# Kernel optimization log

Hardware: AMD Instinct MI355X
Metric: run time of the kernel (lower is better)

Reference implementation:

```python
import jax, jax.numpy as jnp
import numpy as np
import math

EMBED_DIM = 4096
NUM_HEADS = 32
NUM_KV_HEADS = 8
HEAD_DIM = EMBED_DIM // NUM_HEADS          # 128
GROUP_SIZE = NUM_HEADS // NUM_KV_HEADS     # 4
KV_DIM = EMBED_DIM // GROUP_SIZE           # 1024
BATCH, SEQ = 1, 2048


def softermax(x, axis=-1):
    # base-2 softmax with max subtraction (Softermax, arXiv:2103.09301)
    m = jnp.max(x, axis=axis, keepdims=True)
    p = jnp.exp2(x - m)
    return p / jnp.sum(p, axis=axis, keepdims=True)


def setup_inputs() -> dict:
    key = jax.random.key(0)
    ks = jax.random.split(key, 9)
    s = 1.0 / math.sqrt(EMBED_DIM)
    return {
        "x": jax.random.normal(ks[0], (BATCH, SEQ, EMBED_DIM), jnp.float32),
        "q_w": jax.random.normal(ks[1], (EMBED_DIM, EMBED_DIM), jnp.float32) * s,
        "q_b": jax.random.normal(ks[2], (EMBED_DIM,), jnp.float32) * s,
        "k_w": jax.random.normal(ks[3], (KV_DIM, EMBED_DIM), jnp.float32) * s,
        "k_b": jax.random.normal(ks[4], (KV_DIM,), jnp.float32) * s,
        "v_w": jax.random.normal(ks[5], (KV_DIM, EMBED_DIM), jnp.float32) * s,
        "v_b": jax.random.normal(ks[6], (KV_DIM,), jnp.float32) * s,
        "o_w": jax.random.normal(ks[7], (EMBED_DIM, EMBED_DIM), jnp.float32) * s,
        "o_b": jax.random.normal(ks[8], (EMBED_DIM,), jnp.float32) * s,
    }


def reference(x, q_w, q_b, k_w, k_b, v_w, v_b, o_w, o_b):
    B, S, E = x.shape
    # projections (torch Linear: y = x @ W.T + b)
    q = (x @ q_w.T + q_b).reshape(B, S, NUM_HEADS, HEAD_DIM).transpose(0, 2, 1, 3)   # [B,H,S,D]
    k = (x @ k_w.T + k_b).reshape(B, S, NUM_KV_HEADS, HEAD_DIM).transpose(0, 2, 1, 3)  # [B,KV,S,D]
    v = (x @ v_w.T + v_b).reshape(B, S, NUM_KV_HEADS, HEAD_DIM).transpose(0, 2, 1, 3)
    # repeat_kv: expand kv heads to num_heads
    k = jnp.repeat(k, GROUP_SIZE, axis=1)  # [B,H,S,D]
    v = jnp.repeat(v, GROUP_SIZE, axis=1)
    scale = 1.0 / math.sqrt(HEAD_DIM)
    attn = jnp.einsum("bhqd,bhkd->bhqk", q, k * scale)
    attn = softermax(attn, axis=-1)
    out = jnp.einsum("bhqk,bhkd->bhqd", attn, v)
    out = out.transpose(0, 2, 1, 3).reshape(B, S, E)
    return out @ o_w.T + o_b
```

## Files before the change

kernel.cpp:

```cpp
#include <hip/hip_runtime.h>
#include <hip/hip_bf16.h>
#include <stdint.h>

#define SEQL 2048
#define EMB 4096
#define KVDIM 1024
#define HD 128

typedef __attribute__((ext_vector_type(4))) float f32x4;
typedef __attribute__((ext_vector_type(8))) short bf16x8;
typedef unsigned short u16;
typedef unsigned int u32;

__device__ __forceinline__ u16 f2bf(float f) {
  u32 u = __builtin_bit_cast(u32, f);
  u = (u + 0x7FFFu + ((u >> 16) & 1u)) >> 16;
  return (u16)u;
}

__device__ __forceinline__ void gload_lds16(const void* g, void* l) {
  __builtin_amdgcn_global_load_lds(
      (const __attribute__((address_space(1))) void*)g,
      (__attribute__((address_space(3))) void*)l, 16, 0, 0);
}

__global__ __launch_bounds__(256) void k_convert(
    const float* __restrict__ x, const float* __restrict__ qw,
    const float* __restrict__ kw, const float* __restrict__ vw,
    const float* __restrict__ ow, u16* __restrict__ xb, u16* __restrict__ qwb,
    u16* __restrict__ kwb, u16* __restrict__ vwb, u16* __restrict__ owb) {
  const long NCH = 6291456;
  const long stride = (long)gridDim.x * 256;
  for (long c = (long)blockIdx.x * 256 + threadIdx.x; c < NCH; c += stride) {
    long i = c << 3;
    const float* s;
    u16* d;
    long off;
    if (i < 8388608) {
      s = x; d = xb; off = i;
    } else if (i < 25165824) {
      s = qw; d = qwb; off = i - 8388608;
    } else if (i < 29360128) {
      s = kw; d = kwb; off = i - 25165824;
    } else if (i < 33554432) {
      s = vw; d = vwb; off = i - 29360128;
    } else {
      s = ow; d = owb; off = i - 33554432;
    }
    float4 a = *(const float4*)(s + off);
    float4 b = *(const float4*)(s + off + 4);
    bf16x8 o;
    o[0] = f2bf(a.x); o[1] = f2bf(a.y); o[2] = f2bf(a.z); o[3] = f2bf(a.w);
    o[4] = f2bf(b.x); o[5] = f2bf(b.y); o[6] = f2bf(b.z); o[7] = f2bf(b.w);
    *(bf16x8*)(d + off) = o;
  }
}

__device__ __forceinline__ void gemm_128x256(const u16* __restrict__ A,
                                             const u16* __restrict__ B,
                                             long aRow0, long bRow0, int lda,
                                             int ldb, u16* sm, f32x4 acc[4][4]) {
  const int t = threadIdx.x;
  const int lane = t & 63, w = t >> 6;
  const int wr = w >> 2, wc = w & 3;
  const int r15 = lane & 15, hi = lane >> 4;
  const int rsub = lane >> 3;
  const int gofs = ((lane & 7) ^ rsub) << 3;
  const int swz0 = ((0 + hi) ^ (r15 & 7)) << 4;
  const int swz1 = ((4 + hi) ^ (r15 & 7)) << 4;

  auto stage = [&](int buf, int kt) {
    const long k0 = (long)kt * 64 + gofs;
    u16* base = sm + buf * 24576;
#pragma unroll
    for (int i = 0; i < 2; ++i) {
      const int ch = i * 8 + w;
      gload_lds16(A + (aRow0 + ch * 8 + rsub) * (long)lda + k0, base + ch * 512);
    }
#pragma unroll
    for (int i = 0; i < 4; ++i) {
      const int ch = i * 8 + w;
      gload_lds16(B + (bRow0 + ch * 8 + rsub) * (long)ldb + k0,
                  base + 8192 + ch * 512);
    }
  };

  stage(0, 0);
  stage(1, 1);
  asm volatile("s_waitcnt vmcnt(6)" ::: "memory");
  __builtin_amdgcn_s_barrier();

  const char* sc = (const char*)sm;
  int cur = 0;
  for (int kt = 0; kt < 64; ++kt) {
    const char* base = sc + cur * 49152;
    const char* aB = base + (wr * 64 + r15) * 128;
    const char* bB = base + 16384 + (wc * 64 + r15) * 128;
    bf16x8 aF[4][2], bF[2][2];
#pragma unroll
    for (int m = 0; m < 4; ++m) {
      aF[m][0] = *(const bf16x8*)(aB + m * 2048 + swz0);
      aF[m][1] = *(const bf16x8*)(aB + m * 2048 + swz1);
    }
#pragma unroll
    for (int n = 0; n < 2; ++n) {
      bF[n][0] = *(const bf16x8*)(bB + n * 2048 + swz0);
      bF[n][1] = *(const bf16x8*)(bB + n * 2048 + swz1);
    }
    __builtin_amdgcn_s_setprio(1);
#pragma unroll
    for (int m = 0; m < 4; ++m)
#pragma unroll
      for (int n = 0; n < 2; ++n) {
        acc[m][n] = __builtin_amdgcn_mfma_f32_16x16x32_bf16(aF[m][0], bF[n][0],
                                                            acc[m][n], 0, 0, 0);
        acc[m][n] = __builtin_amdgcn_mfma_f32_16x16x32_bf16(aF[m][1], bF[n][1],
                                                            acc[m][n], 0, 0, 0);
      }
    __builtin_amdgcn_s_setprio(0);
    bf16x8 cF[2][2];
#pragma unroll
    for (int n = 0; n < 2; ++n) {
      cF[n][0] = *(const bf16x8*)(bB + (n + 2) * 2048 + swz0);
      cF[n][1] = *(const bf16x8*)(bB + (n + 2) * 2048 + swz1);
    }
    __builtin_amdgcn_s_setprio(1);
#pragma unroll
    for (int m = 0; m < 4; ++m)
#pragma unroll
      for (int n = 0; n < 2; ++n) {
        acc[m][n + 2] = __builtin_amdgcn_mfma_f32_16x16x32_bf16(
            aF[m][0], cF[n][0], acc[m][n + 2], 0, 0, 0);
        acc[m][n + 2] = __builtin_amdgcn_mfma_f32_16x16x32_bf16(
            aF[m][1], cF[n][1], acc[m][n + 2], 0, 0, 0);
      }
    __builtin_amdgcn_s_setprio(0);
    __builtin_amdgcn_s_barrier();
    if (kt + 2 < 64) {
      stage(cur, kt + 2);
      asm volatile("s_waitcnt vmcnt(6)" ::: "memory");
    } else {
      asm volatile("s_waitcnt vmcnt(0)" ::: "memory");
    }
    __builtin_amdgcn_s_barrier();
    cur ^= 1;
  }
}

__global__ __launch_bounds__(512, 2) void k_gemm_qkv(
    const u16* __restrict__ xb, const u16* __restrict__ qwb,
    const u16* __restrict__ kwb, const u16* __restrict__ vwb,
    const float* __restrict__ qb, const float* __restrict__ kb,
    const float* __restrict__ vb, u16* __restrict__ Q, u16* __restrict__ Kc,
    u16* __restrict__ Vt) {
  __shared__ u16 sm[49152];
  const int nt = blockIdx.x, mt = blockIdx.y;
  const u16* W;
  const float* bias;
  long n0;
  int mode;
  if (nt < 16) {
    W = qwb; bias = qb; n0 = (long)nt * 256; mode = 0;
  } else if (nt < 20) {
    W = kwb; bias = kb; n0 = (long)(nt - 16) * 256; mode = 1;
  } else {
    W = vwb; bias = vb; n0 = (long)(nt - 20) * 256; mode = 2;
  }
  const long m0 = (long)mt * 128;
  f32x4 acc[4][4] = {};
  gemm_128x256(xb, W, m0, n0, EMB, EMB, sm, acc);
  const int lane = threadIdx.x & 63, w = threadIdx.x >> 6;
  const int wr = w >> 2, wc = w & 3, r15 = lane & 15, hi = lane >> 4;
#pragma unroll
  for (int n = 0; n < 4; ++n) {
    const long col = n0 + wc * 64 + n * 16 + r15;
    const float bv = bias[col];
#pragma unroll
    for (int m = 0; m < 4; ++m) {
#pragma unroll
      for (int j = 0; j < 4; ++j) {
        const long row = m0 + wr * 64 + m * 16 + hi * 4 + j;
        const float v = acc[m][n][j] + bv;
        if (mode == 0)
          Q[row * EMB + col] = f2bf(v);
        else if (mode == 1)
          Kc[row * KVDIM + col] = f2bf(v);
        else
          Vt[col * SEQL + row] = f2bf(v);
      }
    }
  }
}

__global__ __launch_bounds__(256, 3) void k_attn(const u16* __restrict__ Q,
                                                 const u16* __restrict__ Kc,
                                                 const u16* __restrict__ Vt,
                                                 u16* __restrict__ AO) {
  __shared__ u16 sK[64 * 128];
  __shared__ u16 sV[128 * 64];
  __shared__ u16 sP[4][16 * 72];
  const int h = blockIdx.y, kvh = h >> 2;
  const long q0 = (long)blockIdx.x * 64;
  const int t = threadIdx.x, lane = t & 63, w = t >> 6;
  const int r15 = lane & 15, hi = lane >> 4, kof = hi * 8;
  const float scale = 0.08838834764831845f;

  bf16x8 qf[4];
#pragma unroll
  for (int ks = 0; ks < 4; ++ks)
    qf[ks] = *(const bf16x8*)(Q + (q0 + w * 16 + r15) * EMB + h * HD + ks * 32 + kof);

  f32x4 oacc[8] = {};
  float mx[4], sms[4];
#pragma unroll
  for (int i = 0; i < 4; ++i) {
    mx[i] = -1e30f;
    sms[i] = 0.f;
  }

  for (int tk = 0; tk < 32; ++tk) {
    const long k0 = (long)tk * 64;
    __syncthreads();
#pragma unroll
    for (int i = 0; i < 4; ++i) {
      const int P = (i * 256 + t) * 16;
      const int row = P >> 8;
      const int cb = (P & 255) ^ ((row & 7) << 4);
      gload_lds16(Kc + (k0 + row) * KVDIM + kvh * HD + (cb >> 1),
                  (char*)sK + (i * 256 + w * 64) * 16);
      const int rowv = P >> 7;
      const int cbv = (P & 127) ^ ((rowv & 7) << 4);
      gload_lds16(Vt + (long)(kvh * HD + rowv) * SEQL + k0 + (cbv >> 1),
                  (char*)sV + (i * 256 + w * 64) * 16);
    }
    __syncthreads();
    f32x4 sacc[4] = {};
#pragma unroll
    for (int ks = 0; ks < 4; ++ks) {
      bf16x8 bF[4];
#pragma unroll
      for (int n = 0; n < 4; ++n) {
        const int row = n * 16 + r15;
        const int off = (row << 8) + (((ks * 32 + kof) << 1) ^ ((row & 7) << 4));
        bF[n] = *(const bf16x8*)((const char*)sK + off);
      }
#pragma unroll
      for (int n = 0; n < 4; ++n)
        sacc[n] = __builtin_amdgcn_mfma_f32_16x16x32_bf16(qf[ks], bF[n], sacc[n],
                                                          0, 0, 0);
    }
#pragma unroll
    for (int i = 0; i < 4; ++i) {
      const float pm = fmaxf(fmaxf(sacc[0][i], sacc[1][i]),
                             fmaxf(sacc[2][i], sacc[3][i]));
      if (__any(pm * scale > mx[i] + 8.0f)) {
        float tmax = pm;
#pragma unroll
        for (int msk = 1; msk < 16; msk <<= 1)
          tmax = fmaxf(tmax, __shfl_xor(tmax, msk, 64));
        const float nm = fmaxf(mx[i], tmax * scale);
        const float corr = exp2f(mx[i] - nm);
        mx[i] = nm;
        sms[i] *= corr;
#pragma unroll
        for (int n = 0; n < 8; ++n) oacc[n][i] *= corr;
      }
      float ps = 0.f;
#pragma unroll
      for (int n = 0; n < 4; ++n) {
        const float p = exp2f(sacc[n][i] * scale - mx[i]);
        ps += p;
        sP[w][(hi * 4 + i) * 72 + n * 16 + r15] = f2bf(p);
      }
      sms[i] += ps;
    }
#pragma unroll
    for (int ks = 0; ks < 2; ++ks) {
      const bf16x8 pF = *(const bf16x8*)(&sP[w][r15 * 72 + ks * 32 + kof]);
#pragma unroll
      for (int n = 0; n < 8; ++n) {
        const int row = n * 16 + r15;
        const int off = (row << 7) + (((ks * 32 + kof) << 1) ^ ((row & 7) << 4));
        const bf16x8 vF = *(const bf16x8*)((const char*)sV + off);
        oacc[n] = __builtin_amdgcn_mfma_f32_16x16x32_bf16(pF, vF, oacc[n], 0, 0, 0);
      }
    }
  }
  float inv[4];
#pragma unroll
  for (int i = 0; i < 4; ++i) {
    float s = sms[i];
#pragma unroll
    for (int msk = 1; msk < 16; msk <<= 1) s += __shfl_xor(s, msk, 64);
    inv[i] = 1.f / s;
  }
#pragma unroll
  for (int n = 0; n < 8; ++n)
#pragma unroll
    for (int i = 0; i < 4; ++i)
      AO[(q0 + w * 16 + hi * 4 + i) * EMB + h * HD + n * 16 + r15] =
          f2bf(oacc[n][i] * inv[i]);
}

__global__ __launch_bounds__(512, 2) void k_gemm_o(const u16* __restrict__ AO,
                                                   const u16* __restrict__ owb,
                                                   const float* __restrict__ ob,
                                                   float* __restrict__ OUT) {
  __shared__ u16 sm[49152];
  const long n0 = (long)blockIdx.x * 256, m0 = (long)blockIdx.y * 128;
  f32x4 acc[4][4] = {};
  gemm_128x256(AO, owb, m0, n0, EMB, EMB, sm, acc);
  const int lane = threadIdx.x & 63, w = threadIdx.x >> 6;
  const int wr = w >> 2, wc = w & 3, r15 = lane & 15, hi = lane >> 4;
#pragma unroll
  for (int n = 0; n < 4; ++n) {
    const long col = n0 + wc * 64 + n * 16 + r15;
    const float bv = ob[col];
#pragma unroll
    for (int m = 0; m < 4; ++m) {
#pragma unroll
      for (int j = 0; j < 4; ++j) {
        const long row = m0 + wr * 64 + m * 16 + hi * 4 + j;
        OUT[row * EMB + col] = acc[m][n][j] + bv;
      }
    }
  }
}

extern "C" void kernel_launch(void* const* d_in, const int* in_sizes, int n_in,
                              void* d_out, int out_size, void* d_ws,
                              size_t ws_size, hipStream_t stream) {
  const float* x = (const float*)d_in[0];
  const float* qw = (const float*)d_in[1];
  const float* qb = (const float*)d_in[2];
  const float* kw = (const float*)d_in[3];
  const float* kb = (const float*)d_in[4];
  const float* vw = (const float*)d_in[5];
  const float* vb = (const float*)d_in[6];
  const float* ow = (const float*)d_in[7];
  const float* ob = (const float*)d_in[8];
  float* OUT = (float*)d_out;

  char* ws = (char*)d_ws;
  u16* xb = (u16*)ws;   ws += 16777216;
  u16* qwb = (u16*)ws;  ws += 33554432;
  u16* kwb = (u16*)ws;  ws += 8388608;
  u16* vwb = (u16*)ws;  ws += 8388608;
  u16* owb = (u16*)ws;  ws += 33554432;
  u16* Qb = (u16*)ws;   ws += 16777216;
  u16* Kb = (u16*)ws;   ws += 4194304;
  u16* Vtb = (u16*)ws;  ws += 4194304;
  u16* AO = (u16*)ws;   ws += 16777216;

  k_convert<<<2048, 256, 0, stream>>>(x, qw, kw, vw, ow, xb, qwb, kwb, vwb, owb);
  k_gemm_qkv<<<dim3(24, 16), 512, 0, stream>>>(xb, qwb, kwb, vwb, qb, kb, vb,
                                               Qb, Kb, Vtb);
  k_attn<<<dim3(32, 32), 256, 0, stream>>>(Qb, Kb, Vtb, AO);
  k_gemm_o<<<dim3(16, 16), 512, 0, stream>>>(AO, owb, ob, OUT);
}
```

Measured before the change: 575.0 us.

## Switch projection GEMMs to 256x256 tiles with an 8-phase ping-pong schedule

Replaces the 128x256 double-buffered GEMM core with a 256x256 tile that uses 128KB of LDS. The main loop is split into eight phases that interleave half-tile A/B staging, LDS fragment loads, explicit barriers and waitcnts with MFMA blocks. The aim is more data reuse per tile and better overlap of global loads with matrix math. The cost is fewer workgroups: 192 for the QKV GEMM and 128 for the output GEMM, with one block per CU. That may leave CUs idle on a 256-CU part.

New measurement: 568.7 us. About the same (-1.1%).

```diff
diff --git a/kernel.cpp b/kernel.cpp
--- a/kernel.cpp
+++ b/kernel.cpp
@@ -23,6 +23,15 @@
       (const __attribute__((address_space(1))) void*)g,
       (__attribute__((address_space(3))) void*)l, 16, 0, 0);
 }
+
+#define MFMA16(a, b, c) __builtin_amdgcn_mfma_f32_16x16x32_bf16(a, b, c, 0, 0, 0)
+#define SBAR() asm volatile("s_barrier" ::: "memory")
+#define LGKM0()                                        \
+  do {                                                 \
+    asm volatile("s_waitcnt lgkmcnt(0)" ::: "memory"); \
+    __builtin_amdgcn_sched_barrier(0);                 \
+  } while (0)
+#define VM4() asm volatile("s_waitcnt vmcnt(4)" ::: "memory")
 
 __global__ __launch_bounds__(256) void k_convert(
     const float* __restrict__ x, const float* __restrict__ qw,
@@ -56,94 +65,82 @@
   }
 }
 
-__device__ __forceinline__ void gemm_128x256(const u16* __restrict__ A,
-                                             const u16* __restrict__ B,
-                                             long aRow0, long bRow0, int lda,
-                                             int ldb, u16* sm, f32x4 acc[4][4]) {
-  const int t = threadIdx.x;
-  const int lane = t & 63, w = t >> 6;
+__device__ __forceinline__ void gemm256_8ph(const u16* __restrict__ A,
+                                            const u16* __restrict__ B,
+                                            long aRow0, long bRow0, int lda,
+                                            int ldb, char* lds,
+                                            f32x4 acc[8][4]) {
+  const int t = threadIdx.x, lane = t & 63, w = t >> 6;
   const int wr = w >> 2, wc = w & 3;
   const int r15 = lane & 15, hi = lane >> 4;
   const int rsub = lane >> 3;
   const int gofs = ((lane & 7) ^ rsub) << 3;
-  const int swz0 = ((0 + hi) ^ (r15 & 7)) << 4;
-  const int swz1 = ((4 + hi) ^ (r15 & 7)) << 4;
-
-  auto stage = [&](int buf, int kt) {
+  const int x7 = r15 & 7;
+  const int swz0 = (hi ^ x7) << 4;
+  const int swz1 = ((4 + hi) ^ x7) << 4;
+
+  auto stA = [&](int buf, int half, int kt) {
     const long k0 = (long)kt * 64 + gofs;
-    u16* base = sm + buf * 24576;
-#pragma unroll
-    for (int i = 0; i < 2; ++i) {
-      const int ch = i * 8 + w;
-      gload_lds16(A + (aRow0 + ch * 8 + rsub) * (long)lda + k0, base + ch * 512);
-    }
-#pragma unroll
-    for (int i = 0; i < 4; ++i) {
-      const int ch = i * 8 + w;
-      gload_lds16(B + (bRow0 + ch * 8 + rsub) * (long)ldb + k0,
-                  base + 8192 + ch * 512);
-    }
-  };
-
-  stage(0, 0);
-  stage(1, 1);
-  asm volatile("s_waitcnt vmcnt(6)" ::: "memory");
-  __builtin_amdgcn_s_barrier();
-
-  const char* sc = (const char*)sm;
-  int cur = 0;
-  for (int kt = 0; kt < 64; ++kt) {
-    const char* base = sc + cur * 49152;
-    const char* aB = base + (wr * 64 + r15) * 128;
-    const char* bB = base + 16384 + (wc * 64 + r15) * 128;
-    bf16x8 aF[4][2], bF[2][2];
+    char* dst = lds + buf * 65536 + half * 16384 + w * 1024;
+    const u16* s = A + (aRow0 + half * 128 + w * 8 + rsub) * (long)lda + k0;
+    gload_lds16(s, dst);
+    gload_lds16(s + 64 * (long)lda, dst + 8192);
+  };
+  auto stB = [&](int buf, int half, int kt) {
+    const long k0 = (long)kt * 64 + gofs;
+    char* dst = lds + buf * 65536 + 32768 + half * 16384 + w * 1024;
+    const u16* s = B + (bRow0 + half * 128 + w * 8 + rsub) * (long)ldb + k0;
+    gload_lds16(s, dst);
+    gload_lds16(s + 64 * (long)ldb, dst + 8192);
+  };
+
+  bf16x8 aF[4][2], bF[4][2];
+  auto ldA = [&](int cur, int mh) {
+    const char* p = lds + cur * 65536;
 #pragma unroll
     for (int m = 0; m < 4; ++m) {
-      aF[m][0] = *(const bf16x8*)(aB + m * 2048 + swz0);
-      aF[m][1] = *(const bf16x8*)(aB + m * 2048 + swz1);
-    }
+      const int r = wr * 128 + mh * 64 + m * 16 + r15;
+      aF[m][0] = *(const bf16x8*)(p + r * 128 + swz0);
+      aF[m][1] = *(const bf16x8*)(p + r * 128 + swz1);
+    }
+  };
+  auto ldB = [&](int cur, int nh) {
+    const char* p = lds + cur * 65536 + 32768;
 #pragma unroll
     for (int n = 0; n < 2; ++n) {
-      bF[n][0] = *(const bf16x8*)(bB + n * 2048 + swz0);
-      bF[n][1] = *(const bf16x8*)(bB + n * 2048 + swz1);
-    }
+      const int r = wc * 64 + (nh * 2 + n) * 16 + r15;
+      bF[nh * 2 + n][0] = *(const bf16x8*)(p + r * 128 + swz0);
+      bF[nh * 2 + n][1] = *(const bf16x8*)(p + r * 128 + swz1);
+    }
+  };
+  auto MF = [&](int mh, int nh) {
     __builtin_amdgcn_s_setprio(1);
 #pragma unroll
     for (int m = 0; m < 4; ++m)
 #pragma unroll
       for (int n = 0; n < 2; ++n) {
-        acc[m][n] = __builtin_amdgcn_mfma_f32_16x16x32_bf16(aF[m][0], bF[n][0],
-                                                            acc[m][n], 0, 0, 0);
-        acc[m][n] = __builtin_amdgcn_mfma_f32_16x16x32_bf16(aF[m][1], bF[n][1],
-                                                            acc[m][n], 0, 0, 0);
+        const int am = mh * 4 + m, bn = nh * 2 + n;
+        acc[am][bn] = MFMA16(aF[m][0], bF[bn][0], acc[am][bn]);
+        acc[am][bn] = MFMA16(aF[m][1], bF[bn][1], acc[am][bn]);
       }
     __builtin_amdgcn_s_setprio(0);
-    bf16x8 cF[2][2];
-#pragma unroll
-    for (int n = 0; n < 2; ++n) {
-      cF[n][0] = *(const bf16x8*)(bB + (n + 2) * 2048 + swz0);
-      cF[n][1] = *(const bf16x8*)(bB + (n + 2) * 2048 + swz1);
-    }
-    __builtin_amdgcn_s_setprio(1);
-#pragma unroll
-    for (int m = 0; m < 4; ++m)
-#pragma unroll
-      for (int n = 0; n < 2; ++n) {
-        acc[m][n + 2] = __builtin_amdgcn_mfma_f32_16x16x32_bf16(
-            aF[m][0], cF[n][0], acc[m][n + 2], 0, 0, 0);
-        acc[m][n + 2] = __builtin_amdgcn_mfma_f32_16x16x32_bf16(
-            aF[m][1], cF[n][1], acc[m][n + 2], 0, 0, 0);
-      }
-    __builtin_amdgcn_s_setprio(0);
-    __builtin_amdgcn_s_barrier();
-    if (kt + 2 < 64) {
-      stage(cur, kt + 2);
-      asm volatile("s_waitcnt vmcnt(6)" ::: "memory");
-    } else {
-      asm volatile("s_waitcnt vmcnt(0)" ::: "memory");
-    }
-    __builtin_amdgcn_s_barrier();
-    cur ^= 1;
+  };
+
+  stA(0, 0, 0); stA(0, 1, 0); stB(0, 0, 0); stB(0, 1, 0);
+  stB(1, 0, 1); stB(1, 1, 1);
+  VM4();
+  SBAR();
+
+  for (int i = 0; i < 32; ++i) {
+    const int t1 = (2 * i + 1) & 63, t2 = (2 * i + 2) & 63, t3 = (2 * i + 3) & 63;
+    ldA(0, 0); ldB(0, 0); stA(1, 0, t1); SBAR(); LGKM0(); MF(0, 0); SBAR();
+    ldB(0, 1);            stA(1, 1, t1); SBAR(); LGKM0(); MF(0, 1); SBAR();
+    ldA(0, 1);            stB(0, 0, t2); SBAR(); LGKM0(); MF(1, 0); SBAR();
+                          stB(0, 1, t2); SBAR();          MF(1, 1); VM4(); SBAR();
+    ldA(1, 0); ldB(1, 0); stA(0, 0, t2); SBAR(); LGKM0(); MF(0, 0); SBAR();
+    ldB(1, 1);            stA(0, 1, t2); SBAR(); LGKM0(); MF(0, 1); SBAR();
+    ldA(1, 1);            stB(1, 0, t3); SBAR(); LGKM0(); MF(1, 0); SBAR();
+                          stB(1, 1, t3); SBAR();          MF(1, 1); VM4(); SBAR();
   }
 }
 
@@ -153,7 +150,7 @@
     const float* __restrict__ qb, const float* __restrict__ kb,
     const float* __restrict__ vb, u16* __restrict__ Q, u16* __restrict__ Kc,
     u16* __restrict__ Vt) {
-  __shared__ u16 sm[49152];
+  __shared__ char lds[131072];
   const int nt = blockIdx.x, mt = blockIdx.y;
   const u16* W;
   const float* bias;
@@ -166,9 +163,9 @@
   } else {
     W = vwb; bias = vb; n0 = (long)(nt - 20) * 256; mode = 2;
   }
-  const long m0 = (long)mt * 128;
-  f32x4 acc[4][4] = {};
-  gemm_128x256(xb, W, m0, n0, EMB, EMB, sm, acc);
+  const long m0 = (long)mt * 256;
+  f32x4 acc[8][4] = {};
+  gemm256_8ph(xb, W, m0, n0, EMB, EMB, lds, acc);
   const int lane = threadIdx.x & 63, w = threadIdx.x >> 6;
   const int wr = w >> 2, wc = w & 3, r15 = lane & 15, hi = lane >> 4;
 #pragma unroll
@@ -176,10 +173,10 @@
     const long col = n0 + wc * 64 + n * 16 + r15;
     const float bv = bias[col];
 #pragma unroll
-    for (int m = 0; m < 4; ++m) {
+    for (int m = 0; m < 8; ++m) {
 #pragma unroll
       for (int j = 0; j < 4; ++j) {
-        const long row = m0 + wr * 64 + m * 16 + hi * 4 + j;
+        const long row = m0 + wr * 128 + m * 16 + hi * 4 + j;
         const float v = acc[m][n][j] + bv;
         if (mode == 0)
           Q[row * EMB + col] = f2bf(v);
@@ -246,8 +243,7 @@
       }
 #pragma unroll
       for (int n = 0; n < 4; ++n)
-        sacc[n] = __builtin_amdgcn_mfma_f32_16x16x32_bf16(qf[ks], bF[n], sacc[n],
-                                                          0, 0, 0);
+        sacc[n] = MFMA16(qf[ks], bF[n], sacc[n]);
     }
 #pragma unroll
     for (int i = 0; i < 4; ++i) {
@@ -282,7 +278,7 @@
         const int row = n * 16 + r15;
         const int off = (row << 7) + (((ks * 32 + kof) << 1) ^ ((row & 7) << 4));
         const bf16x8 vF = *(const bf16x8*)((const char*)sV + off);
-        oacc[n] = __builtin_amdgcn_mfma_f32_16x16x32_bf16(pF, vF, oacc[n], 0, 0, 0);
+        oacc[n] = MFMA16(pF, vF, oacc[n]);
       }
     }
   }
@@ -306,10 +302,10 @@
                                                    const u16* __restrict__ owb,
                                                    const float* __restrict__ ob,
                                                    float* __restrict__ OUT) {
-  __shared__ u16 sm[49152];
-  const long n0 = (long)blockIdx.x * 256, m0 = (long)blockIdx.y * 128;
-  f32x4 acc[4][4] = {};
-  gemm_128x256(AO, owb, m0, n0, EMB, EMB, sm, acc);
+  __shared__ char lds[131072];
+  const long n0 = (long)blockIdx.x * 256, m0 = (long)blockIdx.y * 256;
+  f32x4 acc[8][4] = {};
+  gemm256_8ph(AO, owb, m0, n0, EMB, EMB, lds, acc);
   const int lane = threadIdx.x & 63, w = threadIdx.x >> 6;
   const int wr = w >> 2, wc = w & 3, r15 = lane & 15, hi = lane >> 4;
 #pragma unroll
@@ -317,10 +313,10 @@
     const long col = n0 + wc * 64 + n * 16 + r15;
     const float bv = ob[col];
 #pragma unroll
-    for (int m = 0; m < 4; ++m) {
+    for (int m = 0; m < 8; ++m) {
 #pragma unroll
       for (int j = 0; j < 4; ++j) {
-        const long row = m0 + wr * 64 + m * 16 + hi * 4 + j;
+        const long row = m0 + wr * 128 + m * 16 + hi * 4 + j;
         OUT[row * EMB + col] = acc[m][n][j] + bv;
       }
     }
@@ -353,8 +349,8 @@
   u16* AO = (u16*)ws;   ws += 16777216;
 
   k_convert<<<2048, 256, 0, stream>>>(x, qw, kw, vw, ow, xb, qwb, kwb, vwb, owb);
-  k_gemm_qkv<<<dim3(24, 16), 512, 0, stream>>>(xb, qwb, kwb, vwb, qb, kb, vb,
-                                               Qb, Kb, Vtb);
+  k_gemm_qkv<<<dim3(24, 8), 512, 0, stream>>>(xb, qwb, kwb, vwb, qb, kb, vb,
+                                              Qb, Kb, Vtb);
   k_attn<<<dim3(32, 32), 256, 0, stream>>>(Qb, Kb, Vtb, AO);
-  k_gemm_o<<<dim3(16, 16), 512, 0, stream>>>(AO, owb, ob, OUT);
-}
+  k_gemm_o<<<dim3(16, 8), 512, 0, stream>>>(AO, owb, ob, OUT);
+}
```
